# Kernel optimization log

Hardware: AMD Instinct MI355X
Metric: run time of the kernel (lower is better)

## Reference

```python
import jax, jax.numpy as jnp
import numpy as np

B, T, IN, OUT = 8, 2048, 2048, 2048

def setup_inputs() -> dict:
    key = jax.random.key(0)
    k1, k2, k3, k4 = jax.random.split(key, 4)
    x = jax.random.normal(k1, (B, T, IN), dtype=jnp.float32)
    # ternary weights in {-1, 0, 1}, stored as int8 like the torch buffer
    w_q = (jax.random.randint(k2, (OUT, IN), 0, 3) - 1).astype(jnp.int8)
    # per-output-channel power-of-two exponents (downscaling), int8 buffer
    s_exp = jax.random.randint(k3, (OUT,), -8, 1).astype(jnp.int8)
    bias = jax.random.normal(k4, (OUT,), dtype=jnp.float32) * 0.1
    return {"x": x, "w_q": w_q, "s_exp": s_exp, "bias": bias}

def reference(x, w_q, s_exp, bias):
    # F.linear(x, w_q.float()): y[b,t,o] = sum_i x[b,t,i] * w_q[o,i]
    y = jnp.einsum('bti,oi->bto', x, w_q.astype(x.dtype))
    # torch.ldexp(y, s_exp): y * 2**s_exp, broadcast over last dim
    y = y * jnp.exp2(s_exp.astype(jnp.float32)).astype(x.dtype)
    return y + bias
```

## Files before the change

### kernel.cpp

```cpp
#include <hip/hip_runtime.h>

#define MT 16384
#define NT 2048
#define KT 2048
#define BM 256
#define BN 256
#define BK 64
#define NKT (KT / BK)
#define THREADS 512

typedef __attribute__((ext_vector_type(8))) short short8;
typedef __attribute__((ext_vector_type(4))) float f32x4;
typedef __attribute__((ext_vector_type(8))) unsigned short ushort8;
typedef __attribute__((ext_vector_type(4))) unsigned short ushort4v;

__device__ __forceinline__ unsigned short f32_bf16(float f) {
    union { float f; unsigned u; } v; v.f = f;
    return (unsigned short)((v.u + 0x7FFFu + ((v.u >> 16) & 1u)) >> 16);
}


__global__ __launch_bounds__(256) void cvt_kernel(const float* __restrict__ x,
                                                  const int* __restrict__ w,
                                                  unsigned short* __restrict__ xb,
                                                  unsigned short* __restrict__ wb) {
    const int b = blockIdx.x;
    if (b < MT * KT / 2048) {
        size_t i = ((size_t)b * 256 + threadIdx.x) * 8;
        float4 v0 = *(const float4*)(x + i);
        float4 v1 = *(const float4*)(x + i + 4);
        ushort8 o;
        o[0] = f32_bf16(v0.x); o[1] = f32_bf16(v0.y); o[2] = f32_bf16(v0.z); o[3] = f32_bf16(v0.w);
        o[4] = f32_bf16(v1.x); o[5] = f32_bf16(v1.y); o[6] = f32_bf16(v1.z); o[7] = f32_bf16(v1.w);
        *(ushort8*)(xb + i) = o;
    } else {
        size_t i = ((size_t)(b - MT * KT / 2048) * 256 + threadIdx.x) * 8;
        int4 v0 = *(const int4*)(w + i);
        int4 v1 = *(const int4*)(w + i + 4);
        ushort8 o;
        o[0] = f32_bf16((float)v0.x); o[1] = f32_bf16((float)v0.y);
        o[2] = f32_bf16((float)v0.z); o[3] = f32_bf16((float)v0.w);
        o[4] = f32_bf16((float)v1.x); o[5] = f32_bf16((float)v1.y);
        o[6] = f32_bf16((float)v1.z); o[7] = f32_bf16((float)v1.w);
        *(ushort8*)(wb + i) = o;
    }
}


__global__ __launch_bounds__(THREADS, 2) void gemm_8ph(
    const unsigned short* __restrict__ Abf, const unsigned short* __restrict__ Bbf,
    const int* __restrict__ sexp, const float* __restrict__ bias,
    float* __restrict__ C)
{
    __shared__ unsigned short As[2 * 2048 * 8];
    __shared__ unsigned short Bs[2 * 2048 * 8];

    const int tid  = threadIdx.x;
    const int bn   = blockIdx.x;
    const int bm   = blockIdx.y;
    const int brow0 = bm * BM;
    const int bcol0 = bn * BN;
    const int lane = tid & 63;
    const int wave = tid >> 6;
    const int wm = wave >> 2;
    const int wn = wave & 3;
    const int q = lane >> 4, r = lane & 15;

    size_t aoff[2][2], boff[2][2];
    #pragma unroll
    for (int h = 0; h < 2; ++h)
        #pragma unroll
        for (int ii = 0; ii < 2; ++ii) {
            const int s   = h * 1024 + ii * 512 + tid;
            const int row = s >> 3;
            const int cg  = ((s & 7) - row) & 7;
            aoff[h][ii] = (size_t)(brow0 + row) * KT + cg * 8;
            boff[h][ii] = (size_t)(bcol0 + row) * KT + cg * 8;
        }

#define GLDS(srcp, dstp)                                                            \
    __builtin_amdgcn_global_load_lds(                                               \
        (const __attribute__((address_space(1))) unsigned int*)(srcp),              \
        (__attribute__((address_space(3))) unsigned int*)(dstp), 16, 0, 0)

    auto stageA = [&](int tile, int h) {
        const int buf = tile & 1;
        const size_t k = (size_t)tile * BK;
        GLDS(Abf + aoff[h][0] + k, As + buf * 16384 + (h * 1024 + wave * 64) * 8);
        GLDS(Abf + aoff[h][1] + k, As + buf * 16384 + (h * 1024 + 512 + wave * 64) * 8);
    };
    auto stageB = [&](int tile, int h) {
        const int buf = tile & 1;
        const size_t k = (size_t)tile * BK;
        GLDS(Bbf + boff[h][0] + k, Bs + buf * 16384 + (h * 1024 + wave * 64) * 8);
        GLDS(Bbf + boff[h][1] + k, Bs + buf * 16384 + (h * 1024 + 512 + wave * 64) * 8);
    };

    f32x4 acc[8][4] = {};
    short8 a[2][2];
    short8 b[4][2];

    auto ldA = [&](int buf, int p) {
        const unsigned short* base = As + buf * 16384;
        #pragma unroll
        for (int u = 0; u < 2; ++u) {
            const int row = (4 * p + 2 * u + wm) * 16 + r;
            #pragma unroll
            for (int kh = 0; kh < 2; ++kh)
                a[u][kh] = *(const short8*)(base + row * 64 + ((kh * 4 + q + row) & 7) * 8);
        }
    };
    auto ldB = [&](int buf) {
        const unsigned short* base = Bs + buf * 16384;
        #pragma unroll
        for (int j = 0; j < 4; ++j) {
            const int row = (4 * wn + j) * 16 + r;
            #pragma unroll
            for (int kh = 0; kh < 2; ++kh)
                b[j][kh] = *(const short8*)(base + row * 64 + ((kh * 4 + q + row) & 7) * 8);
        }
    };
    auto mma = [&](int p) {
        #pragma unroll
        for (int kh = 0; kh < 2; ++kh)
            #pragma unroll
            for (int u = 0; u < 2; ++u)
                #pragma unroll
                for (int j = 0; j < 4; ++j)
                    acc[2 * p + u][j] = __builtin_amdgcn_mfma_f32_16x16x32_bf16(
                        a[u][kh], b[j][kh], acc[2 * p + u][j], 0, 0, 0);
    };

#define PHASE(buf, p, STAGE_STMT, WAIT_STMT) do {          \
        ldA(buf, p);                                       \
        if ((p) == 0) ldB(buf);                            \
        STAGE_STMT;                                        \
        __builtin_amdgcn_s_barrier();                      \
        asm volatile("s_waitcnt lgkmcnt(0)");              \
        __builtin_amdgcn_sched_barrier(0);                 \
        __builtin_amdgcn_s_setprio(1);                     \
        mma(p);                                            \
        __builtin_amdgcn_s_setprio(0);                     \
        WAIT_STMT;                                         \
        __builtin_amdgcn_s_barrier();                      \
    } while (0)

    stageB(0, 0); stageB(0, 1); stageA(0, 0); stageA(0, 1);
    asm volatile("s_waitcnt vmcnt(4)" ::: "memory");
    stageB(1, 0); stageA(1, 0); stageB(1, 1);
    asm volatile("s_waitcnt vmcnt(6)" ::: "memory");
    __builtin_amdgcn_s_barrier();

    #pragma unroll 1
    for (int i = 0; i < NKT / 2 - 1; ++i) {
        const int t1 = 2 * i + 1, t2 = 2 * i + 2, t3 = 2 * i + 3;
        PHASE(0, 0, stageA(t1, 1), (void)0);
        PHASE(0, 1, stageB(t2, 0), (void)0);
        PHASE(0, 2, stageA(t2, 0), (void)0);
        PHASE(0, 3, stageB(t2, 1), asm volatile("s_waitcnt vmcnt(6)" ::: "memory"));
        PHASE(1, 0, stageA(t2, 1), (void)0);
        PHASE(1, 1, stageB(t3, 0), (void)0);
        PHASE(1, 2, stageA(t3, 0), (void)0);
        PHASE(1, 3, stageB(t3, 1), asm volatile("s_waitcnt vmcnt(6)" ::: "memory"));
    }

    PHASE(0, 0, stageA(NKT - 1, 1), (void)0);
    PHASE(0, 1, (void)0, asm volatile("s_waitcnt vmcnt(4)" ::: "memory"));
    PHASE(0, 2, (void)0, asm volatile("s_waitcnt vmcnt(2)" ::: "memory"));
    PHASE(0, 3, (void)0, asm volatile("s_waitcnt vmcnt(0)" ::: "memory"));
    PHASE(1, 0, (void)0, (void)0);
    PHASE(1, 1, (void)0, (void)0);
    PHASE(1, 2, (void)0, (void)0);
    PHASE(1, 3, (void)0, (void)0);

#undef PHASE
#undef GLDS

    #pragma unroll
    for (int j = 0; j < 4; ++j) {
        const int n  = bcol0 + (4 * wn + j) * 16 + r;
        const float sc = ldexpf(1.0f, sexp[n]);
        const float bs = bias[n];
        #pragma unroll
        for (int f = 0; f < 8; ++f) {
            const int m = brow0 + (2 * f + wm) * 16 + q * 4;
            float* cp = C + (size_t)m * NT + n;
            #pragma unroll
            for (int t = 0; t < 4; ++t)
                cp[(size_t)t * NT] = acc[f][j][t] * sc + bs;
        }
    }
}


__device__ __forceinline__ int swzf(int row, int c) { return row * 8 + ((c + row) & 7); }

__global__ __launch_bounds__(256) void gemm_fb(
    const float* __restrict__ Af32, const int* __restrict__ Wi32,
    const int* __restrict__ sexp, const float* __restrict__ bias,
    float* __restrict__ C)
{
    __shared__ unsigned short As[128 * 64];
    __shared__ unsigned short Bs[128 * 64];

    const int tid  = threadIdx.x;
    const int row0 = blockIdx.y * 128;
    const int col0 = blockIdx.x * 128;
    const int lane = tid & 63;
    const int wave = tid >> 6;
    const int wm = wave >> 1, wn = wave & 1;
    const int q = lane >> 4, r = lane & 15;

    f32x4 acc[4][4] = {};

    for (int k0 = 0; k0 < KT; k0 += 64) {
        #pragma unroll
        for (int ii = 0; ii < 8; ++ii) {
            const int s  = tid + ii * 256;
            const int rw = s >> 4, c4 = s & 15;
            const int ch = c4 >> 1, hf = c4 & 1;
            const int ps = ((ch + rw) & 7) * 8 + hf * 4;
            float4 v = *(const float4*)(Af32 + (size_t)(row0 + rw) * KT + k0 + c4 * 4);
            ushort4v oa;
            oa[0] = f32_bf16(v.x); oa[1] = f32_bf16(v.y);
            oa[2] = f32_bf16(v.z); oa[3] = f32_bf16(v.w);
            *(ushort4v*)(As + rw * 64 + ps) = oa;
            int4 w4 = *(const int4*)(Wi32 + (size_t)(col0 + rw) * KT + k0 + c4 * 4);
            ushort4v ob;
            ob[0] = f32_bf16((float)w4.x); ob[1] = f32_bf16((float)w4.y);
            ob[2] = f32_bf16((float)w4.z); ob[3] = f32_bf16((float)w4.w);
            *(ushort4v*)(Bs + rw * 64 + ps) = ob;
        }
        __syncthreads();
        #pragma unroll
        for (int h = 0; h < 2; ++h) {
            short8 a[4], b[4];
            #pragma unroll
            for (int i = 0; i < 4; ++i)
                a[i] = *(const short8*)(As + swzf(wm * 64 + i * 16 + r, h * 4 + q) * 8);
            #pragma unroll
            for (int j = 0; j < 4; ++j)
                b[j] = *(const short8*)(Bs + swzf(wn * 64 + j * 16 + r, h * 4 + q) * 8);
            #pragma unroll
            for (int i = 0; i < 4; ++i)
                #pragma unroll
                for (int j = 0; j < 4; ++j)
                    acc[i][j] = __builtin_amdgcn_mfma_f32_16x16x32_bf16(a[i], b[j], acc[i][j], 0, 0, 0);
        }
        __syncthreads();
    }

    #pragma unroll
    for (int j = 0; j < 4; ++j) {
        const int n  = col0 + wn * 64 + j * 16 + r;
        const float sc = ldexpf(1.0f, sexp[n]);
        const float bs = bias[n];
        #pragma unroll
        for (int i = 0; i < 4; ++i) {
            const int m = row0 + wm * 64 + i * 16 + q * 4;
            float* cp = C + (size_t)m * NT + n;
            #pragma unroll
            for (int t = 0; t < 4; ++t)
                cp[(size_t)t * NT] = acc[i][j][t] * sc + bs;
        }
    }
}

extern "C" void kernel_launch(void* const* d_in, const int* in_sizes, int n_in,
                              void* d_out, int out_size, void* d_ws, size_t ws_size,
                              hipStream_t stream) {
    const float* x    = (const float*)d_in[0];
    const int*   wq   = (const int*)d_in[1];
    const int*   se   = (const int*)d_in[2];
    const float* bias = (const float*)d_in[3];
    float* out = (float*)d_out;

    const size_t xb_elems = (size_t)MT * KT;
    const size_t wb_elems = (size_t)NT * KT;

    if (ws_size >= (xb_elems + wb_elems) * sizeof(unsigned short)) {
        unsigned short* xb = (unsigned short*)d_ws;
        unsigned short* wb = xb + xb_elems;
        cvt_kernel<<<(int)((xb_elems + wb_elems) / (256 * 8)), 256, 0, stream>>>(x, wq, xb, wb);
        dim3 grid(NT / BN, MT / BM);
        gemm_8ph<<<grid, THREADS, 0, stream>>>(xb, wb, se, bias, out);
    } else {
        dim3 fgrid(NT / 128, MT / 128);
        gemm_fb<<<fgrid, 256, 0, stream>>>(x, wq, se, bias, out);
    }
}
```

Baseline: 364.5 us.

## Switch GEMM inner loop from 16x16x32 to 32x32x16 bf16 MFMA

Replaces the 16x16x32 bf16 MFMA tiling with 32x32x16 MFMA. Each wave now covers its 64x128 per-phase sub-tile with 2x2 larger blocks instead of 4x4 small ones. The LDS fragment loads, accumulator layout and epilogue row/column mapping are rewritten to match the 32x32 output layout. The goal is fewer MFMA issues and fewer LDS reads per FLOP, since the larger instruction has better operand reuse. The cost is a different register footprint and a less coalesced epilogue store pattern.

```diff
diff --git a/kernel.cpp b/kernel.cpp
--- a/kernel.cpp
+++ b/kernel.cpp
@@ -10,6 +10,7 @@
 #define THREADS 512
 
 typedef __attribute__((ext_vector_type(8))) short short8;
+typedef __attribute__((ext_vector_type(16))) float f32x16;
 typedef __attribute__((ext_vector_type(4))) float f32x4;
 typedef __attribute__((ext_vector_type(8))) unsigned short ushort8;
 typedef __attribute__((ext_vector_type(4))) unsigned short ushort4v;
@@ -64,7 +65,8 @@
     const int wave = tid >> 6;
     const int wm = wave >> 2;
     const int wn = wave & 3;
-    const int q = lane >> 4, r = lane & 15;
+    const int l31 = lane & 31;
+    const int hi  = lane >> 5;
 
     size_t aoff[2][2], boff[2][2];
     #pragma unroll
@@ -96,39 +98,36 @@
         GLDS(Bbf + boff[h][1] + k, Bs + buf * 16384 + (h * 1024 + 512 + wave * 64) * 8);
     };
 
-    f32x4 acc[8][4] = {};
-    short8 a[2][2];
-    short8 b[4][2];
+    f32x16 acc[4][2] = {};
+    short8 a[4];
+    short8 b[2][4];
 
     auto ldA = [&](int buf, int p) {
         const unsigned short* base = As + buf * 16384;
-        #pragma unroll
-        for (int u = 0; u < 2; ++u) {
-            const int row = (4 * p + 2 * u + wm) * 16 + r;
-            #pragma unroll
-            for (int kh = 0; kh < 2; ++kh)
-                a[u][kh] = *(const short8*)(base + row * 64 + ((kh * 4 + q + row) & 7) * 8);
+        const int row = (2 * p + wm) * 32 + l31;
+        #pragma unroll
+        for (int kh = 0; kh < 4; ++kh) {
+            const int c = kh * 2 + hi;
+            a[kh] = *(const short8*)(base + row * 64 + ((c + row) & 7) * 8);
         }
     };
     auto ldB = [&](int buf) {
         const unsigned short* base = Bs + buf * 16384;
         #pragma unroll
-        for (int j = 0; j < 4; ++j) {
-            const int row = (4 * wn + j) * 16 + r;
-            #pragma unroll
-            for (int kh = 0; kh < 2; ++kh)
-                b[j][kh] = *(const short8*)(base + row * 64 + ((kh * 4 + q + row) & 7) * 8);
+        for (int j = 0; j < 2; ++j) {
+            const int row = (wn * 2 + j) * 32 + l31;
+            #pragma unroll
+            for (int kh = 0; kh < 4; ++kh)
+                b[j][kh] = *(const short8*)(base + row * 64 + ((kh * 2 + hi + row) & 7) * 8);
         }
     };
     auto mma = [&](int p) {
         #pragma unroll
-        for (int kh = 0; kh < 2; ++kh)
-            #pragma unroll
-            for (int u = 0; u < 2; ++u)
-                #pragma unroll
-                for (int j = 0; j < 4; ++j)
-                    acc[2 * p + u][j] = __builtin_amdgcn_mfma_f32_16x16x32_bf16(
-                        a[u][kh], b[j][kh], acc[2 * p + u][j], 0, 0, 0);
+        for (int kh = 0; kh < 4; ++kh)
+            #pragma unroll
+            for (int j = 0; j < 2; ++j)
+                acc[p][j] = __builtin_amdgcn_mfma_f32_32x32x16_bf16(
+                    a[kh], b[j][kh], acc[p][j], 0, 0, 0);
     };
 
 #define PHASE(buf, p, STAGE_STMT, WAIT_STMT) do {          \
@@ -177,17 +176,18 @@
 #undef GLDS
 
     #pragma unroll
-    for (int j = 0; j < 4; ++j) {
-        const int n  = bcol0 + (4 * wn + j) * 16 + r;
+    for (int j = 0; j < 2; ++j) {
+        const int n  = bcol0 + (wn * 2 + j) * 32 + l31;
         const float sc = ldexpf(1.0f, sexp[n]);
         const float bs = bias[n];
         #pragma unroll
-        for (int f = 0; f < 8; ++f) {
-            const int m = brow0 + (2 * f + wm) * 16 + q * 4;
-            float* cp = C + (size_t)m * NT + n;
-            #pragma unroll
-            for (int t = 0; t < 4; ++t)
-                cp[(size_t)t * NT] = acc[f][j][t] * sc + bs;
+        for (int f = 0; f < 4; ++f) {
+            const int mbase = brow0 + (2 * f + wm) * 32 + hi * 4;
+            #pragma unroll
+            for (int reg = 0; reg < 16; ++reg) {
+                const int m = mbase + (reg & 3) + 8 * (reg >> 2);
+                C[(size_t)m * NT + n] = acc[f][j][reg] * sc + bs;
+            }
         }
     }
 }
```

After: 379.1 us. +4.0%, slower.

## Restructure GEMM inner loop to k-half phases with batched prefetch stages

Applied to the files above, without the earlier changes.

Splits each 64-wide k tile into two k-halves and two M-quarter phases, so each phase loads four A fragments and four B fragments (B only on the first quarter) and issues 16 MFMAs over a single k-half. Register fragments shrink from 2x2 A plus 4x2 B to 4 A plus 4 B. The global-to-LDS staging schedule changes: one A half is staged early in a tile, then both B halves and the first A half of tile+2 are issued together in the last phase. This is meant to lower register pressure and rebalance LDS reads against MFMA work, at the cost of more B reloads per tile and a different latency-hiding pattern.

```diff
diff --git a/kernel.cpp b/kernel.cpp
--- a/kernel.cpp
+++ b/kernel.cpp
@@ -97,88 +97,86 @@
     };
 
     f32x4 acc[8][4] = {};
-    short8 a[2][2];
-    short8 b[4][2];
-
-    auto ldA = [&](int buf, int p) {
+    short8 a[4];
+    short8 b[4];
+
+    auto ldA = [&](int buf, int fq, int kh) {
         const unsigned short* base = As + buf * 16384;
         #pragma unroll
-        for (int u = 0; u < 2; ++u) {
-            const int row = (4 * p + 2 * u + wm) * 16 + r;
-            #pragma unroll
-            for (int kh = 0; kh < 2; ++kh)
-                a[u][kh] = *(const short8*)(base + row * 64 + ((kh * 4 + q + row) & 7) * 8);
-        }
-    };
-    auto ldB = [&](int buf) {
+        for (int u = 0; u < 4; ++u) {
+            const int row = (2 * (fq * 4 + u) + wm) * 16 + r;
+            a[u] = *(const short8*)(base + row * 64 + ((kh * 4 + q + row) & 7) * 8);
+        }
+    };
+    auto ldB = [&](int buf, int kh) {
         const unsigned short* base = Bs + buf * 16384;
         #pragma unroll
         for (int j = 0; j < 4; ++j) {
-            const int row = (4 * wn + j) * 16 + r;
-            #pragma unroll
-            for (int kh = 0; kh < 2; ++kh)
-                b[j][kh] = *(const short8*)(base + row * 64 + ((kh * 4 + q + row) & 7) * 8);
-        }
-    };
-    auto mma = [&](int p) {
-        #pragma unroll
-        for (int kh = 0; kh < 2; ++kh)
-            #pragma unroll
-            for (int u = 0; u < 2; ++u)
-                #pragma unroll
-                for (int j = 0; j < 4; ++j)
-                    acc[2 * p + u][j] = __builtin_amdgcn_mfma_f32_16x16x32_bf16(
-                        a[u][kh], b[j][kh], acc[2 * p + u][j], 0, 0, 0);
-    };
-
-#define PHASE(buf, p, STAGE_STMT, WAIT_STMT) do {          \
-        ldA(buf, p);                                       \
-        if ((p) == 0) ldB(buf);                            \
+            const int row = wn * 64 + j * 16 + r;
+            b[j] = *(const short8*)(base + row * 64 + ((kh * 4 + q + row) & 7) * 8);
+        }
+    };
+    auto mma = [&](int fq) {
+        #pragma unroll
+        for (int u = 0; u < 4; ++u)
+            #pragma unroll
+            for (int j = 0; j < 4; ++j)
+                acc[fq * 4 + u][j] = __builtin_amdgcn_mfma_f32_16x16x32_bf16(
+                    a[u], b[j], acc[fq * 4 + u][j], 0, 0, 0);
+    };
+
+#define PHASE(buf, fq, kh, STAGE_STMT, WAIT_STMT) do {     \
+        ldA(buf, fq, kh);                                  \
+        if ((fq) == 0) ldB(buf, kh);                       \
         STAGE_STMT;                                        \
         __builtin_amdgcn_s_barrier();                      \
         asm volatile("s_waitcnt lgkmcnt(0)");              \
         __builtin_amdgcn_sched_barrier(0);                 \
         __builtin_amdgcn_s_setprio(1);                     \
-        mma(p);                                            \
+        mma(fq);                                           \
         __builtin_amdgcn_s_setprio(0);                     \
         WAIT_STMT;                                         \
         __builtin_amdgcn_s_barrier();                      \
     } while (0)
 
+#define TILE(buf, t, PH0_STAGE, PH3_STAGE, PH3_WAIT) do {  \
+        PHASE(buf, 0, 0, PH0_STAGE, (void)0);              \
+        PHASE(buf, 1, 0, (void)0,   (void)0);              \
+        PHASE(buf, 0, 1, (void)0,   (void)0);              \
+        PHASE(buf, 1, 1, PH3_STAGE, PH3_WAIT);             \
+    } while (0)
+
     stageB(0, 0); stageB(0, 1); stageA(0, 0); stageA(0, 1);
-    asm volatile("s_waitcnt vmcnt(4)" ::: "memory");
-    stageB(1, 0); stageA(1, 0); stageB(1, 1);
+    stageB(1, 0); stageB(1, 1); stageA(1, 0);
     asm volatile("s_waitcnt vmcnt(6)" ::: "memory");
     __builtin_amdgcn_s_barrier();
 
     #pragma unroll 1
-    for (int i = 0; i < NKT / 2 - 1; ++i) {
-        const int t1 = 2 * i + 1, t2 = 2 * i + 2, t3 = 2 * i + 3;
-        PHASE(0, 0, stageA(t1, 1), (void)0);
-        PHASE(0, 1, stageB(t2, 0), (void)0);
-        PHASE(0, 2, stageA(t2, 0), (void)0);
-        PHASE(0, 3, stageB(t2, 1), asm volatile("s_waitcnt vmcnt(6)" ::: "memory"));
-        PHASE(1, 0, stageA(t2, 1), (void)0);
-        PHASE(1, 1, stageB(t3, 0), (void)0);
-        PHASE(1, 2, stageA(t3, 0), (void)0);
-        PHASE(1, 3, stageB(t3, 1), asm volatile("s_waitcnt vmcnt(6)" ::: "memory"));
-    }
-
-    PHASE(0, 0, stageA(NKT - 1, 1), (void)0);
-    PHASE(0, 1, (void)0, asm volatile("s_waitcnt vmcnt(4)" ::: "memory"));
-    PHASE(0, 2, (void)0, asm volatile("s_waitcnt vmcnt(2)" ::: "memory"));
-    PHASE(0, 3, (void)0, asm volatile("s_waitcnt vmcnt(0)" ::: "memory"));
-    PHASE(1, 0, (void)0, (void)0);
-    PHASE(1, 1, (void)0, (void)0);
-    PHASE(1, 2, (void)0, (void)0);
-    PHASE(1, 3, (void)0, (void)0);
-
+    for (int i = 0; i < 15; ++i) {
+        const int t0 = 2 * i, t1 = 2 * i + 1;
+        TILE(0, t0,
+             { stageA(t0 + 1, 1); },
+             { stageB(t0 + 2, 0); stageB(t0 + 2, 1); stageA(t0 + 2, 0); },
+             asm volatile("s_waitcnt vmcnt(6)" ::: "memory"));
+        TILE(1, t1,
+             { stageA(t1 + 1, 1); },
+             { stageB(t1 + 2, 0); stageB(t1 + 2, 1); stageA(t1 + 2, 0); },
+             asm volatile("s_waitcnt vmcnt(6)" ::: "memory"));
+    }
+
+    TILE(0, 30,
+         { stageA(31, 1); },
+         (void)0,
+         asm volatile("s_waitcnt vmcnt(0)" ::: "memory"));
+    TILE(1, 31, (void)0, (void)0, (void)0);
+
+#undef TILE
 #undef PHASE
 #undef GLDS
 
     #pragma unroll
     for (int j = 0; j < 4; ++j) {
-        const int n  = bcol0 + (4 * wn + j) * 16 + r;
+        const int n  = bcol0 + wn * 64 + j * 16 + r;
         const float sc = ldexpf(1.0f, sexp[n]);
         const float bs = bias[n];
         #pragma unroll
```

Measured after the change: 370.0 us. No clear change (+1.5%).
